# Performance work log

Hardware: AMD Instinct MI355X
Metric: run time of the kernel (lower is better)

## Reference

```python
import jax, jax.numpy as jnp
import numpy as np

MAX_SPAN = 16
EPS = 1e-12


def setup_inputs() -> dict:
    key = jax.random.key(0)
    ks = jax.random.split(key, 10)
    B, S, H, R = 64, 512, 768, 51
    embed = jax.random.normal(ks[0], (B, S, H), dtype=jnp.float32)
    sub_head = jax.random.randint(ks[1], (B,), 0, S - MAX_SPAN, dtype=jnp.int32)
    span = jax.random.randint(ks[2], (B,), 0, MAX_SPAN, dtype=jnp.int32)
    sub_tail = sub_head + span  # guaranteed valid span inside [0, S)
    s = 0.02
    W_ih = jax.random.normal(ks[3], (4 * H, H), dtype=jnp.float32) * s
    W_hh = jax.random.normal(ks[4], (4 * H, H), dtype=jnp.float32) * s
    b_ih = jnp.zeros((4 * H,), dtype=jnp.float32)
    b_hh = jnp.zeros((4 * H,), dtype=jnp.float32)
    cln_weight = jnp.ones((H,), dtype=jnp.float32)
    cln_bias = jnp.zeros((H,), dtype=jnp.float32)
    # nonzero so the conditional path is exercised (init is zeros in torch)
    cln_Ww = jax.random.normal(ks[5], (H, H), dtype=jnp.float32) * s
    cln_Wb = jax.random.normal(ks[6], (H, H), dtype=jnp.float32) * s
    Wh = jax.random.normal(ks[7], (R, H), dtype=jnp.float32) * s
    bh = jnp.zeros((R,), dtype=jnp.float32)
    Wt = jax.random.normal(ks[8], (R, H), dtype=jnp.float32) * s
    bt = jnp.zeros((R,), dtype=jnp.float32)
    return {"embed": embed, "sub_head": sub_head, "sub_tail": sub_tail,
            "W_ih": W_ih, "W_hh": W_hh, "b_ih": b_ih, "b_hh": b_hh,
            "cln_weight": cln_weight, "cln_bias": cln_bias,
            "cln_Ww": cln_Ww, "cln_Wb": cln_Wb,
            "Wh": Wh, "bh": bh, "Wt": Wt, "bt": bt}


def _ragged_lstm(embed, sub_head, sub_tail, W_ih, W_hh, b_ih, b_hh):
    # Pack ragged spans [head, tail] into a padded [B, MAX_SPAN, H] block and
    # run one batched LSTM scan, freezing state once past each span's end.
    B, S, H = embed.shape
    offs = jnp.arange(MAX_SPAN, dtype=sub_head.dtype)
    pos = sub_head[:, None] + offs[None, :]                    # [B, T]
    idx = jnp.clip(pos, 0, S - 1)
    x = jnp.take_along_axis(embed, idx[:, :, None], axis=1)    # [B, T, H]
    mask = pos <= sub_tail[:, None]                            # [B, T]

    def step(carry, inp):
        h, c = carry
        xt, mt = inp                                           # [B,H], [B]
        gates = xt @ W_ih.T + b_ih + h @ W_hh.T + b_hh         # [B, 4H]
        i, f, g, o = jnp.split(gates, 4, axis=-1)
        c_new = jax.nn.sigmoid(f) * c + jax.nn.sigmoid(i) * jnp.tanh(g)
        h_new = jax.nn.sigmoid(o) * jnp.tanh(c_new)
        m = mt[:, None]
        h = jnp.where(m, h_new, h)
        c = jnp.where(m, c_new, c)
        return (h, c), None

    h0 = jnp.zeros((B, H), dtype=embed.dtype)
    (hn, _), _ = jax.lax.scan(step, (h0, h0),
                              (x.transpose(1, 0, 2), mask.T))
    return hn                                                  # [B, H]


def _cond_layernorm(inputs, cond, weight, bias, Ww, Wb):
    # weight/bias are conditioned on `cond` via zero-init dense layers
    w = cond @ Ww.T + weight                                   # [B, H]
    b = cond @ Wb.T + bias
    mu = jnp.mean(inputs, axis=-1, keepdims=True)
    xc = inputs - mu
    var = jnp.mean(xc * xc, axis=-1, keepdims=True)
    std = jnp.sqrt(var + EPS)
    return w[:, None, :] * xc / (std + EPS) + b[:, None, :]


def reference(embed, sub_head, sub_tail, W_ih, W_hh, b_ih, b_hh,
              cln_weight, cln_bias, cln_Ww, cln_Wb, Wh, bh, Wt, bt):
    sub_embed = _ragged_lstm(embed, sub_head, sub_tail, W_ih, W_hh, b_ih, b_hh)
    new_embed = _cond_layernorm(embed, sub_embed, cln_weight, cln_bias,
                                cln_Ww, cln_Wb)
    heads = jax.nn.sigmoid(new_embed @ Wh.T + bh)              # [B, S, R]
    tails = jax.nn.sigmoid(new_embed @ Wt.T + bt)
    return heads, tails
```

## Files before the change

kernel.cpp:

```cpp
#include <hip/hip_runtime.h>

typedef __attribute__((ext_vector_type(8))) short bhalf8;
typedef __attribute__((ext_vector_type(4))) float floatx4;

__device__ unsigned short g_whh[3072*768];
__device__ unsigned short g_whl[128*768];
__device__ unsigned short g_h2[2*64*768];
__device__ float g_cbuf[64*768];
__device__ unsigned short g_xg[16*64*3072];
__device__ float g_wv[64*768], g_bv[64*768];
__device__ float g_bias[3072];
__device__ float g_cw[768], g_cb[768];
__device__ float g_bh[64], g_bt[64];

static __device__ __forceinline__ unsigned short f2bf(float f){
  unsigned u = __builtin_bit_cast(unsigned, f);
  u = (u + 0x7FFFu + ((u >> 16) & 1u)) >> 16;
  return (unsigned short)u;
}
static __device__ __forceinline__ float bf2f(unsigned short v){
  unsigned u = ((unsigned)v) << 16;
  return __builtin_bit_cast(float, u);
}
static __device__ __forceinline__ float sigm(float x){ return 1.0f/(1.0f + __expf(-x)); }
static __device__ __forceinline__ float tanhq(float x){ float e = __expf(-2.0f*x); return (1.0f - e)/(1.0f + e); }

static __device__ __forceinline__ uint4 pk8(const float* __restrict__ s){
  float4 a = ((const float4*)s)[0];
  float4 b = ((const float4*)s)[1];
  uint4 v;
  v.x = (unsigned)f2bf(a.x) | ((unsigned)f2bf(a.y) << 16);
  v.y = (unsigned)f2bf(a.z) | ((unsigned)f2bf(a.w) << 16);
  v.z = (unsigned)f2bf(b.x) | ((unsigned)f2bf(b.y) << 16);
  v.w = (unsigned)f2bf(b.z) | ((unsigned)f2bf(b.w) << 16);
  return v;
}

__global__ __launch_bounds__(256) void casrel_prep(
    const float* __restrict__ W_hh,
    const float* __restrict__ Wh,   const float* __restrict__ Wt,
    const float* __restrict__ b_ih, const float* __restrict__ b_hh,
    const float* __restrict__ cw,   const float* __restrict__ cb,
    const float* __restrict__ bh,   const float* __restrict__ bt){
  const long CW = 294912;
  const long CL = 12288;
  const long CH = 12288;
  const long CF = 6144;
  const long CB = 384, CV = 96, CR = 8;
  const long total = CW + CL + CH + CF + CB + CV*2 + CR*2;
  for(long i = (long)blockIdx.x*256 + threadIdx.x; i < total; i += (long)gridDim.x*256){
    long j = i;
    if(j < CW){ *(uint4*)(g_whh + j*8) = pk8(W_hh + j*8); continue; } j -= CW;
    if(j < CL){ long e = j*8;
                long r = e / 768, k = e - r*768;
                if(r < 51)       *(uint4*)(g_whl + e) = pk8(Wh + r*768 + k);
                else if(r < 102) *(uint4*)(g_whl + e) = pk8(Wt + (r-51)*768 + k);
                else             *(uint4*)(g_whl + e) = make_uint4(0,0,0,0);
                continue; } j -= CL;
    if(j < CH){ *(uint4*)(g_h2 + j*8) = make_uint4(0,0,0,0); continue; } j -= CH;
    if(j < CF){ long e = j*8;
                *(float4*)(g_cbuf + e)     = make_float4(0,0,0,0);
                *(float4*)(g_cbuf + e + 4) = make_float4(0,0,0,0);
                continue; } j -= CF;
    if(j < CB){ long e = j*8;
                #pragma unroll
                for(int q=0;q<8;q++) g_bias[e+q] = b_ih[e+q] + b_hh[e+q];
                continue; } j -= CB;
    if(j < CV){ long e = j*8;
                *(float4*)(g_cw + e)     = *(const float4*)(cw + e);
                *(float4*)(g_cw + e + 4) = *(const float4*)(cw + e + 4);
                continue; } j -= CV;
    if(j < CV){ long e = j*8;
                *(float4*)(g_cb + e)     = *(const float4*)(cb + e);
                *(float4*)(g_cb + e + 4) = *(const float4*)(cb + e + 4);
                continue; } j -= CV;
    if(j < CR){ long e = j*8;
                #pragma unroll
                for(int q=0;q<8;q++){ long n = e+q; g_bh[n] = (n < 51) ? bh[n] : 0.0f; }
                continue; } j -= CR;
    { long e = j*8;
      #pragma unroll
      for(int q=0;q<8;q++){ long n = e+q; g_bt[n] = (n < 51) ? bt[n] : 0.0f; } }
  }
}

__global__ __launch_bounds__(256) void casrel_xgates(
    const float* __restrict__ embed, const int* __restrict__ head,
    const float* __restrict__ W_ih){
  __shared__ char sB[128*128];
  const int tid = threadIdx.x, l = tid & 63, w = tid >> 6;
  const int n0 = blockIdx.x * 128;
  const int m0 = blockIdx.y * 64 + w*16;
  const int mrow = m0 + (l & 15);
  const int b = mrow >> 4, t = mrow & 15;
  int pos = head[b] + t; pos = pos < 0 ? 0 : (pos > 511 ? 511 : pos);
  const float* aptr = embed + ((long)b*512 + pos)*768 + ((l >> 4)*8);
  floatx4 acc[8];
  #pragma unroll
  for(int q=0;q<8;q++){ acc[q][0]=0.f; acc[q][1]=0.f; acc[q][2]=0.f; acc[q][3]=0.f; }
  for(int kt=0; kt<12; ++kt){
    __syncthreads();
    #pragma unroll
    for(int j=0;j<4;j++){
      int f = tid + 256*j;
      int row = f >> 3, seg = f & 7;
      uint4 v = pk8(W_ih + ((long)(n0+row))*768 + kt*64 + seg*8);
      *(uint4*)(sB + row*128 + ((seg*16) ^ ((row & 7) << 4))) = v;
    }
    __syncthreads();
    #pragma unroll
    for(int ks=0; ks<2; ++ks){
      const int k = kt*64 + ks*32;
      float4 lo = *(const float4*)(aptr + k);
      float4 hi = *(const float4*)(aptr + k + 4);
      bhalf8 a;
      a[0]=(short)f2bf(lo.x); a[1]=(short)f2bf(lo.y); a[2]=(short)f2bf(lo.z); a[3]=(short)f2bf(lo.w);
      a[4]=(short)f2bf(hi.x); a[5]=(short)f2bf(hi.y); a[6]=(short)f2bf(hi.z); a[7]=(short)f2bf(hi.w);
      const int kb = ks*64 + ((l >> 4)*16);
      #pragma unroll
      for(int q=0;q<8;q++){
        int row = q*16 + (l & 15);
        bhalf8 bb = *(const bhalf8*)(sB + row*128 + (kb ^ ((row & 7) << 4)));
        acc[q] = __builtin_amdgcn_mfma_f32_16x16x32_bf16(a, bb, acc[q], 0, 0, 0);
      }
    }
  }
  #pragma unroll
  for(int q=0;q<8;q++){
    const int n = n0 + q*16 + (l & 15);
    const float bias = g_bias[n];
    #pragma unroll
    for(int r=0;r<4;r++){
      const int m = m0 + (l >> 4)*4 + r;
      const int bb2 = m >> 4, tt = m & 15;
      g_xg[((long)(tt*64 + bb2))*3072 + n] = f2bf(acc[q][r] + bias);
    }
  }
}

__global__ __launch_bounds__(256) void casrel_step(
    const int* __restrict__ head, const int* __restrict__ tail, int t){
  __shared__ char sW[32*1536];
  const unsigned short* hin = g_h2 + (t & 1)*49152;
  unsigned short* hout = g_h2 + ((t & 1) ^ 1)*49152;
  const int tid = threadIdx.x, l = tid & 63, w = tid >> 6;
  const int j0 = blockIdx.x * 8;
  #pragma unroll
  for(int j=0;j<12;j++){
    int f = tid + 256*j;
    int row = f / 96, seg = f - row*96;
    int grow = (row >> 3)*768 + j0 + (row & 7);
    uint4 v = *(const uint4*)(g_whh + (long)grow*768 + seg*8);
    *(uint4*)(sW + row*1536 + ((seg*16) ^ ((row & 7) << 4))) = v;
  }
  __syncthreads();
  const int arow = w*16 + (l & 15);
  floatx4 acc[2];
  #pragma unroll
  for(int q=0;q<2;q++){ acc[q][0]=0.f; acc[q][1]=0.f; acc[q][2]=0.f; acc[q][3]=0.f; }
  const unsigned short* ap = hin + arow*768 + ((l >> 4)*8);
  #pragma unroll 6
  for(int ks=0; ks<24; ++ks){
    bhalf8 a = *(const bhalf8*)(ap + ks*32);
    const int kb = ks*64 + ((l >> 4)*16);
    #pragma unroll
    for(int q=0;q<2;q++){
      int row = q*16 + (l & 15);
      bhalf8 bb = *(const bhalf8*)(sW + row*1536 + (kb ^ ((row & 7) << 4)));
      acc[q] = __builtin_amdgcn_mfma_f32_16x16x32_bf16(a, bb, acc[q], 0, 0, 0);
    }
  }
  const int c = l & 7;
  const int jown = j0 + c;
  const bool lo = (l & 8) == 0;
  #pragma unroll
  for(int r=0;r<4;r++){
    const int b = w*16 + (l >> 4)*4 + r;
    float v0 = acc[0][r], v1 = acc[1][r];
    float o0 = __shfl_xor(v0, 8);
    float o1 = __shfl_xor(v1, 8);
    if(lo){
      const int cell = b*768 + jown;
      const unsigned short* xp = g_xg + ((long)(t*64 + b))*3072 + jown;
      float Gi = v0 + bf2f(xp[0]);
      float Gf = o0 + bf2f(xp[768]);
      float Gg = v1 + bf2f(xp[1536]);
      float Go = o1 + bf2f(xp[2304]);
      if(t <= tail[b] - head[b]){
        float cc = g_cbuf[cell];
        float ig = sigm(Gi), fg = sigm(Gf), gg = tanhq(Gg), og = sigm(Go);
        cc = fg*cc + ig*gg;
        g_cbuf[cell] = cc;
        hout[cell] = f2bf(og*tanhq(cc));
      } else {
        hout[cell] = hin[cell];
      }
    }
  }
}

__global__ __launch_bounds__(256) void casrel_clnproj(
    const float* __restrict__ Ww, const float* __restrict__ Wb){
  __shared__ char sW[32*1536];
  const int tid = threadIdx.x, l = tid & 63, w = tid >> 6;
  const int n0c = blockIdx.x * 32;
  #pragma unroll
  for(int j=0;j<12;j++){
    int f = tid + 256*j;
    int row = f / 96, seg = f - row*96;
    const int n = n0c + row;
    uint4 v = (n < 768) ? pk8(Ww + (long)n*768 + seg*8)
                        : pk8(Wb + (long)(n-768)*768 + seg*8);
    *(uint4*)(sW + row*1536 + ((seg*16) ^ ((row & 7) << 4))) = v;
  }
  __syncthreads();
  const int arow = w*16 + (l & 15);
  floatx4 acc2[2];
  #pragma unroll
  for(int q=0;q<2;q++){ acc2[q][0]=0.f; acc2[q][1]=0.f; acc2[q][2]=0.f; acc2[q][3]=0.f; }
  const unsigned short* ap2 = g_h2 + arow*768 + ((l >> 4)*8);
  for(int ks=0; ks<24; ++ks){
    bhalf8 a = *(const bhalf8*)(ap2 + ks*32);
    const int kb = ks*64 + ((l >> 4)*16);
    #pragma unroll
    for(int q=0;q<2;q++){
      int row = q*16 + (l & 15);
      bhalf8 bb = *(const bhalf8*)(sW + row*1536 + (kb ^ ((row & 7) << 4)));
      acc2[q] = __builtin_amdgcn_mfma_f32_16x16x32_bf16(a, bb, acc2[q], 0, 0, 0);
    }
  }
  #pragma unroll
  for(int q=0;q<2;q++){
    const int n = n0c + q*16 + (l & 15);
    #pragma unroll
    for(int r=0;r<4;r++){
      const int b = w*16 + (l >> 4)*4 + r;
      float v = acc2[q][r];
      if(n < 768) g_wv[b*768 + n] = v + g_cw[n];
      else        g_bv[b*768 + (n - 768)] = v + g_cb[n - 768];
    }
  }
}

__global__ __launch_bounds__(256) void casrel_out(
    const float* __restrict__ embed, float* __restrict__ out){
  __shared__ char sB[128*128];
  __shared__ char sE[32*128];
  __shared__ float sMu[32], sRs[32];
  const int tid = threadIdx.x, l = tid & 63, w = tid >> 6;
  const int b = blockIdx.y;
  const int s0 = blockIdx.x * 32;
  const float* xbase = embed + ((long)b*512 + s0)*768;
  for(int rr=0; rr<8; ++rr){
    const int row = w*8 + rr;
    const float* rp = xbase + row*768;
    float sm = 0.f, sq = 0.f;
    #pragma unroll
    for(int q=0;q<3;q++){
      float4 v = *(const float4*)(rp + l*4 + q*256);
      sm += v.x + v.y + v.z + v.w;
      sq += v.x*v.x + v.y*v.y + v.z*v.z + v.w*v.w;
    }
    #pragma unroll
    for(int o=32;o>0;o>>=1){ sm += __shfl_xor(sm, o); sq += __shfl_xor(sq, o); }
    if(l == 0){
      float mu = sm * (1.0f/768.0f);
      float var = sq * (1.0f/768.0f) - mu*mu;
      sMu[row] = mu;
      sRs[row] = 1.0f/(sqrtf(var + 1e-12f) + 1e-12f);
    }
  }
  __syncthreads();
  const int mf = w >> 1, nb = (w & 1)*4;
  floatx4 acc[4];
  #pragma unroll
  for(int q=0;q<4;q++){ acc[q][0]=0.f; acc[q][1]=0.f; acc[q][2]=0.f; acc[q][3]=0.f; }
  for(int kt=0; kt<12; ++kt){
    __syncthreads();
    #pragma unroll
    for(int j=0;j<4;j++){
      int f = tid + 256*j;
      int row = f >> 3, seg = f & 7;
      uint4 v = *(const uint4*)(g_whl + (long)row*768 + kt*64 + seg*8);
      *(uint4*)(sB + row*128 + ((seg*16) ^ ((row & 7) << 4))) = v;
    }
    #pragma unroll
    for(int j=0;j<2;j++){
      int f = tid + 256*j;
      int row = f >> 4, cs = f & 15;
      int k = kt*64 + cs*4;
      float4 x4 = *(const float4*)(xbase + row*768 + k);
      float4 w4 = *(const float4*)(g_wv + b*768 + k);
      float4 c4 = *(const float4*)(g_bv + b*768 + k);
      float mu = sMu[row], rs = sRs[row];
      unsigned long long pk =
          (unsigned long long)f2bf((x4.x - mu)*rs*w4.x + c4.x)
        | ((unsigned long long)f2bf((x4.y - mu)*rs*w4.y + c4.y) << 16)
        | ((unsigned long long)f2bf((x4.z - mu)*rs*w4.z + c4.z) << 32)
        | ((unsigned long long)f2bf((x4.w - mu)*rs*w4.w + c4.w) << 48);
      *(unsigned long long*)(sE + row*128 + ((cs*8) ^ ((row & 7) << 4))) = pk;
    }
    __syncthreads();
    #pragma unroll
    for(int ks=0; ks<2; ++ks){
      const int arow = mf*16 + (l & 15);
      const int kb = ks*64 + ((l >> 4)*16);
      bhalf8 a = *(const bhalf8*)(sE + arow*128 + (kb ^ ((arow & 7) << 4)));
      #pragma unroll
      for(int q=0;q<4;q++){
        int row = (nb + q)*16 + (l & 15);
        bhalf8 bb = *(const bhalf8*)(sB + row*128 + (kb ^ ((row & 7) << 4)));
        acc[q] = __builtin_amdgcn_mfma_f32_16x16x32_bf16(a, bb, acc[q], 0, 0, 0);
      }
    }
  }
  const long HT = (long)64*512*51;
  #pragma unroll
  for(int q=0;q<4;q++){
    const int n = (nb + q)*16 + (l & 15);
    if(n >= 102) continue;
    const int rr = (n < 51) ? n : (n - 51);
    const long obase = (n < 51) ? 0 : HT;
    const float bias = (n < 51) ? g_bh[n] : g_bt[n - 51];
    #pragma unroll
    for(int r=0;r<4;r++){
      const int s = s0 + mf*16 + (l >> 4)*4 + r;
      out[obase + ((long)b*512 + s)*51 + rr] = sigm(acc[q][r] + bias);
    }
  }
}

extern "C" void kernel_launch(void* const* d_in, const int* in_sizes, int n_in,
                              void* d_out, int out_size, void* d_ws, size_t ws_size,
                              hipStream_t stream){
  const float* embed = (const float*)d_in[0];
  const int*   head  = (const int*)d_in[1];
  const int*   tail  = (const int*)d_in[2];
  const float* W_ih  = (const float*)d_in[3];
  const float* W_hh  = (const float*)d_in[4];
  const float* b_ih  = (const float*)d_in[5];
  const float* b_hh  = (const float*)d_in[6];
  const float* cw    = (const float*)d_in[7];
  const float* cb    = (const float*)d_in[8];
  const float* Ww    = (const float*)d_in[9];
  const float* Wb    = (const float*)d_in[10];
  const float* Wh    = (const float*)d_in[11];
  const float* bh    = (const float*)d_in[12];
  const float* Wt    = (const float*)d_in[13];
  const float* bt    = (const float*)d_in[14];
  float* out = (float*)d_out;
  (void)d_ws; (void)ws_size;

  casrel_prep<<<dim3(1024), dim3(256), 0, stream>>>(W_hh, Wh, Wt, b_ih, b_hh, cw, cb, bh, bt);
  casrel_xgates<<<dim3(24,16), dim3(256), 0, stream>>>(embed, head, W_ih);
  for(int t=0; t<16; ++t)
    casrel_step<<<dim3(96), dim3(256), 0, stream>>>(head, tail, t);
  casrel_clnproj<<<dim3(48), dim3(256), 0, stream>>>(Ww, Wb);
  casrel_out<<<dim3(16,64), dim3(256), 0, stream>>>(embed, out);
}
```

Measured before the change: 247.1 us.

## Fuse LSTM timesteps and CLN projection into one cooperative persistent kernel

Replaces the 16 per-timestep launches plus the separate conditional-layernorm projection launch with a single cooperative kernel. W_hh tiles stay resident in LDS across steps, and steps are separated by a grid-wide sync instead of kernel boundaries. It also folds the bias sum into the x-gates kernel, dropping that work from prep. The gain is fewer launches and no reloading of weights each step, at the cost of grid barriers and the requirement that all 96 blocks be co-resident.

```diff
diff --git a/kernel.cpp b/kernel.cpp
--- a/kernel.cpp
+++ b/kernel.cpp
@@ -1,4 +1,7 @@
 #include <hip/hip_runtime.h>
+#include <hip/hip_cooperative_groups.h>
+
+namespace cg = cooperative_groups;
 
 typedef __attribute__((ext_vector_type(8))) short bhalf8;
 typedef __attribute__((ext_vector_type(4))) float floatx4;
@@ -9,7 +12,6 @@
 __device__ float g_cbuf[64*768];
 __device__ unsigned short g_xg[16*64*3072];
 __device__ float g_wv[64*768], g_bv[64*768];
-__device__ float g_bias[3072];
 __device__ float g_cw[768], g_cb[768];
 __device__ float g_bh[64], g_bt[64];
 
@@ -39,15 +41,14 @@
 __global__ __launch_bounds__(256) void casrel_prep(
     const float* __restrict__ W_hh,
     const float* __restrict__ Wh,   const float* __restrict__ Wt,
-    const float* __restrict__ b_ih, const float* __restrict__ b_hh,
     const float* __restrict__ cw,   const float* __restrict__ cb,
     const float* __restrict__ bh,   const float* __restrict__ bt){
   const long CW = 294912;
   const long CL = 12288;
   const long CH = 12288;
   const long CF = 6144;
-  const long CB = 384, CV = 96, CR = 8;
-  const long total = CW + CL + CH + CF + CB + CV*2 + CR*2;
+  const long CV = 96, CR = 8;
+  const long total = CW + CL + CH + CF + CV*2 + CR*2;
   for(long i = (long)blockIdx.x*256 + threadIdx.x; i < total; i += (long)gridDim.x*256){
     long j = i;
     if(j < CW){ *(uint4*)(g_whh + j*8) = pk8(W_hh + j*8); continue; } j -= CW;
@@ -62,10 +63,6 @@
                 *(float4*)(g_cbuf + e)     = make_float4(0,0,0,0);
                 *(float4*)(g_cbuf + e + 4) = make_float4(0,0,0,0);
                 continue; } j -= CF;
-    if(j < CB){ long e = j*8;
-                #pragma unroll
-                for(int q=0;q<8;q++) g_bias[e+q] = b_ih[e+q] + b_hh[e+q];
-                continue; } j -= CB;
     if(j < CV){ long e = j*8;
                 *(float4*)(g_cw + e)     = *(const float4*)(cw + e);
                 *(float4*)(g_cw + e + 4) = *(const float4*)(cw + e + 4);
@@ -86,7 +83,8 @@
 
 __global__ __launch_bounds__(256) void casrel_xgates(
     const float* __restrict__ embed, const int* __restrict__ head,
-    const float* __restrict__ W_ih){
+    const float* __restrict__ W_ih,
+    const float* __restrict__ b_ih, const float* __restrict__ b_hh){
   __shared__ char sB[128*128];
   const int tid = threadIdx.x, l = tid & 63, w = tid >> 6;
   const int n0 = blockIdx.x * 128;
@@ -128,7 +126,7 @@
   #pragma unroll
   for(int q=0;q<8;q++){
     const int n = n0 + q*16 + (l & 15);
-    const float bias = g_bias[n];
+    const float bias = b_ih[n] + b_hh[n];
     #pragma unroll
     for(int r=0;r<4;r++){
       const int m = m0 + (l >> 4)*4 + r;
@@ -138,11 +136,11 @@
   }
 }
 
-__global__ __launch_bounds__(256) void casrel_step(
-    const int* __restrict__ head, const int* __restrict__ tail, int t){
+__global__ __launch_bounds__(256) void casrel_lstm(
+    const int* __restrict__ head, const int* __restrict__ tail,
+    const float* __restrict__ Ww, const float* __restrict__ Wb){
   __shared__ char sW[32*1536];
-  const unsigned short* hin = g_h2 + (t & 1)*49152;
-  unsigned short* hout = g_h2 + ((t & 1) ^ 1)*49152;
+  cg::grid_group grid = cg::this_grid();
   const int tid = threadIdx.x, l = tid & 63, w = tid >> 6;
   const int j0 = blockIdx.x * 8;
   #pragma unroll
@@ -155,54 +153,62 @@
   }
   __syncthreads();
   const int arow = w*16 + (l & 15);
-  floatx4 acc[2];
-  #pragma unroll
-  for(int q=0;q<2;q++){ acc[q][0]=0.f; acc[q][1]=0.f; acc[q][2]=0.f; acc[q][3]=0.f; }
-  const unsigned short* ap = hin + arow*768 + ((l >> 4)*8);
-  #pragma unroll 6
-  for(int ks=0; ks<24; ++ks){
-    bhalf8 a = *(const bhalf8*)(ap + ks*32);
-    const int kb = ks*64 + ((l >> 4)*16);
-    #pragma unroll
-    for(int q=0;q<2;q++){
-      int row = q*16 + (l & 15);
-      bhalf8 bb = *(const bhalf8*)(sW + row*1536 + (kb ^ ((row & 7) << 4)));
-      acc[q] = __builtin_amdgcn_mfma_f32_16x16x32_bf16(a, bb, acc[q], 0, 0, 0);
-    }
-  }
   const int c = l & 7;
   const int jown = j0 + c;
   const bool lo = (l & 8) == 0;
+  int spown[4];
   #pragma unroll
   for(int r=0;r<4;r++){
-    const int b = w*16 + (l >> 4)*4 + r;
-    float v0 = acc[0][r], v1 = acc[1][r];
-    float o0 = __shfl_xor(v0, 8);
-    float o1 = __shfl_xor(v1, 8);
-    if(lo){
-      const int cell = b*768 + jown;
-      const unsigned short* xp = g_xg + ((long)(t*64 + b))*3072 + jown;
-      float Gi = v0 + bf2f(xp[0]);
-      float Gf = o0 + bf2f(xp[768]);
-      float Gg = v1 + bf2f(xp[1536]);
-      float Go = o1 + bf2f(xp[2304]);
-      if(t <= tail[b] - head[b]){
-        float cc = g_cbuf[cell];
-        float ig = sigm(Gi), fg = sigm(Gf), gg = tanhq(Gg), og = sigm(Go);
-        cc = fg*cc + ig*gg;
-        g_cbuf[cell] = cc;
-        hout[cell] = f2bf(og*tanhq(cc));
-      } else {
-        hout[cell] = hin[cell];
+    int b = w*16 + (l >> 4)*4 + r;
+    spown[r] = tail[b] - head[b];
+  }
+  for(int t=0;t<16;t++){
+    const unsigned short* hin = g_h2 + (t & 1)*49152;
+    unsigned short* hout = g_h2 + ((t & 1) ^ 1)*49152;
+    floatx4 acc[2];
+    #pragma unroll
+    for(int q=0;q<2;q++){ acc[q][0]=0.f; acc[q][1]=0.f; acc[q][2]=0.f; acc[q][3]=0.f; }
+    const unsigned short* ap = hin + arow*768 + ((l >> 4)*8);
+    #pragma unroll 6
+    for(int ks=0; ks<24; ++ks){
+      bhalf8 a = *(const bhalf8*)(ap + ks*32);
+      const int kb = ks*64 + ((l >> 4)*16);
+      #pragma unroll
+      for(int q=0;q<2;q++){
+        int row = q*16 + (l & 15);
+        bhalf8 bb = *(const bhalf8*)(sW + row*1536 + (kb ^ ((row & 7) << 4)));
+        acc[q] = __builtin_amdgcn_mfma_f32_16x16x32_bf16(a, bb, acc[q], 0, 0, 0);
       }
     }
-  }
-}
-
-__global__ __launch_bounds__(256) void casrel_clnproj(
-    const float* __restrict__ Ww, const float* __restrict__ Wb){
-  __shared__ char sW[32*1536];
-  const int tid = threadIdx.x, l = tid & 63, w = tid >> 6;
+    #pragma unroll
+    for(int r=0;r<4;r++){
+      const int b = w*16 + (l >> 4)*4 + r;
+      float v0 = acc[0][r], v1 = acc[1][r];
+      float o0 = __shfl_xor(v0, 8);
+      float o1 = __shfl_xor(v1, 8);
+      if(lo){
+        const int cell = b*768 + jown;
+        const unsigned short* xp = g_xg + ((long)(t*64 + b))*3072 + jown;
+        float Gi = v0 + bf2f(xp[0]);
+        float Gf = o0 + bf2f(xp[768]);
+        float Gg = v1 + bf2f(xp[1536]);
+        float Go = o1 + bf2f(xp[2304]);
+        if(t <= spown[r]){
+          float cc = g_cbuf[cell];
+          float ig = sigm(Gi), fg = sigm(Gf), gg = tanhq(Gg), og = sigm(Go);
+          cc = fg*cc + ig*gg;
+          g_cbuf[cell] = cc;
+          hout[cell] = f2bf(og*tanhq(cc));
+        } else {
+          hout[cell] = hin[cell];
+        }
+      }
+    }
+    __threadfence();
+    grid.sync();
+  }
+  if(blockIdx.x >= 48) return;
+  __syncthreads();
   const int n0c = blockIdx.x * 32;
   #pragma unroll
   for(int j=0;j<12;j++){
@@ -214,7 +220,6 @@
     *(uint4*)(sW + row*1536 + ((seg*16) ^ ((row & 7) << 4))) = v;
   }
   __syncthreads();
-  const int arow = w*16 + (l & 15);
   floatx4 acc2[2];
   #pragma unroll
   for(int q=0;q<2;q++){ acc2[q][0]=0.f; acc2[q][1]=0.f; acc2[q][2]=0.f; acc2[q][3]=0.f; }
@@ -351,10 +356,11 @@
   float* out = (float*)d_out;
   (void)d_ws; (void)ws_size;
 
-  casrel_prep<<<dim3(1024), dim3(256), 0, stream>>>(W_hh, Wh, Wt, b_ih, b_hh, cw, cb, bh, bt);
-  casrel_xgates<<<dim3(24,16), dim3(256), 0, stream>>>(embed, head, W_ih);
-  for(int t=0; t<16; ++t)
-    casrel_step<<<dim3(96), dim3(256), 0, stream>>>(head, tail, t);
-  casrel_clnproj<<<dim3(48), dim3(256), 0, stream>>>(Ww, Wb);
+  casrel_prep<<<dim3(1024), dim3(256), 0, stream>>>(W_hh, Wh, Wt, cw, cb, bh, bt);
+  casrel_xgates<<<dim3(24,16), dim3(256), 0, stream>>>(embed, head, W_ih, b_ih, b_hh);
+  {
+    void* args[] = {(void*)&head, (void*)&tail, (void*)&Ww, (void*)&Wb};
+    hipLaunchCooperativeKernel((void*)casrel_lstm, dim3(96), dim3(256), args, 0, stream);
+  }
   casrel_out<<<dim3(16,64), dim3(256), 0, stream>>>(embed, out);
 }
```

After: 577.7 us. +133.8%, slower.
